# Kernel optimization log

Measured on AMD Instinct MI355X. Metric: run time of the kernel, lower is better.

## Reference

```python
import math
import jax, jax.numpy as jnp
import numpy as np

B, S, D = 4, 2048, 1024
H, HD = 16, 64
NUM_BUCKETS = 32
MAX_DISTANCE = 128
EPS = 1e-6
ENC_S = 512


def _relative_position_bucket(relative_position):
    # bidirectional=False path
    num_buckets = NUM_BUCKETS
    rp = -jnp.minimum(relative_position, 0)  # [S, S] nonneg
    max_exact = num_buckets // 2
    is_small = rp < max_exact
    scale = (num_buckets - max_exact) / math.log(MAX_DISTANCE / max_exact)
    large = max_exact + (jnp.log(jnp.maximum(rp, 1).astype(jnp.float32) / max_exact) * scale).astype(jnp.int32)
    large = jnp.minimum(large, num_buckets - 1)
    return jnp.where(is_small, rp, large)


def compute_bias(rel_emb, q_len, k_len):
    ctx = jnp.arange(q_len)[:, None]
    mem = jnp.arange(k_len)[None, :]
    bucket = _relative_position_bucket(mem - ctx)          # [q, k] int
    values = rel_emb[bucket]                                # [q, k, H]
    return jnp.transpose(values, (2, 0, 1))[None]           # [1, H, q, k]


def setup_inputs() -> dict:
    key = jax.random.key(0)
    ks = jax.random.split(key, 8)
    std = 0.02
    return {
        "input_ids": jax.random.normal(ks[0], (B, S, D), jnp.float32),
        "encoder_output": jax.random.normal(ks[1], (B, ENC_S, D), jnp.float32),
        "wq": jax.random.normal(ks[2], (D, H * HD), jnp.float32) * std,
        "wk": jax.random.normal(ks[3], (D, H * HD), jnp.float32) * std,
        "wv": jax.random.normal(ks[4], (D, H * HD), jnp.float32) * std,
        "wo": jax.random.normal(ks[5], (H * HD, D), jnp.float32) * std,
        "rel_emb": jax.random.normal(ks[6], (NUM_BUCKETS, H), jnp.float32) * std,
        "ln_w": jnp.ones((D,), jnp.float32),
    }


def reference(input_ids, encoder_output, wq, wk, wv, wo, rel_emb, ln_w):
    origin = input_ids
    # MT5LayerNorm: RMS norm, no mean subtraction, no bias
    variance = jnp.mean(jnp.square(input_ids.astype(jnp.float32)), axis=-1, keepdims=True)
    x = (input_ids * jax.lax.rsqrt(variance + EPS)) * ln_w

    q = (x @ wq).reshape(B, S, H, HD)
    k = (x @ wk).reshape(B, S, H, HD)
    v = (x @ wv).reshape(B, S, H, HD)

    # NOTE: T5-style attention has no 1/sqrt(d) scaling
    scores = jnp.einsum("bqhd,bkhd->bhqk", q, k)
    scores = scores + compute_bias(rel_emb, S, S)
    attn = jax.nn.softmax(scores, axis=-1)
    ctx = jnp.einsum("bhqk,bkhd->bqhd", attn, v).reshape(B, S, H * HD)
    attn_out = ctx @ wo

    # residual connection (dropout is identity at rate 0 / eval)
    return origin + attn_out
```

## Files before the change

### kernel.cpp

```cpp
#include <hip/hip_runtime.h>
#include <hip/hip_bf16.h>
#include <math.h>

#define S_LEN 2048
#define D_DIM 1024
#define NHEAD 16

typedef __attribute__((ext_vector_type(8))) short bf16x8;
typedef __attribute__((ext_vector_type(4))) float floatx4;

__device__ __forceinline__ short f32_bf16(float f) {
  union { float f; unsigned u; } v; v.f = f;
  unsigned r = v.u + 0x7FFFu + ((v.u >> 16) & 1u);
  return (short)(r >> 16);
}

__device__ __forceinline__ float exp2_fast(float x) {
#if __has_builtin(__builtin_amdgcn_exp2f)
  return __builtin_amdgcn_exp2f(x);
#else
  float r; asm("v_exp_f32 %0, %1" : "=v"(r) : "v"(x)); return r;
#endif
}

__device__ __forceinline__ void gload16(const void* g, void* l) {
  __builtin_amdgcn_global_load_lds((const __attribute__((address_space(1))) unsigned*)g,
                                   (__attribute__((address_space(3))) unsigned*)l,
                                   16, 0, 0);
}

__global__ __launch_bounds__(256) void prep_k(const float* __restrict__ x,
                                              const float* __restrict__ lnw,
                                              const float* __restrict__ wq,
                                              const float* __restrict__ wk,
                                              const float* __restrict__ wv,
                                              const float* __restrict__ wo,
                                              short* __restrict__ xb,
                                              short* __restrict__ oqkv,
                                              short* __restrict__ owo) {
  if (blockIdx.x < 8192) {
    int row = blockIdx.x;
    const float4* xr = (const float4*)(x + (size_t)row * D_DIM);
    float4 v = xr[threadIdx.x];
    float ss = v.x*v.x + v.y*v.y + v.z*v.z + v.w*v.w;
    #pragma unroll
    for (int off = 32; off > 0; off >>= 1) ss += __shfl_xor(ss, off);
    __shared__ float red[4];
    if ((threadIdx.x & 63) == 0) red[threadIdx.x >> 6] = ss;
    __syncthreads();
    float scale = rsqrtf((red[0]+red[1]+red[2]+red[3]) * (1.f/D_DIM) + 1e-6f);
    float4 wv4 = ((const float4*)lnw)[threadIdx.x];
    short4 o;
    o.x = f32_bf16(v.x*scale*wv4.x);
    o.y = f32_bf16(v.y*scale*wv4.y);
    o.z = f32_bf16(v.z*scale*wv4.z);
    o.w = f32_bf16(v.w*scale*wv4.w);
    ((short4*)xb)[(size_t)row*256 + threadIdx.x] = o;
  } else {
    int t = (blockIdx.x - 8192)*256 + threadIdx.x;
    if (t < 3072*1024) {
      int n = t >> 10, k = t & 1023;
      const float* src = (n < 1024) ? wq : ((n < 2048) ? wk : wv);
      float scale = (n < 1024) ? 1.44269504f : 1.0f;
      oqkv[t] = f32_bf16(src[(size_t)k*1024 + (n & 1023)] * scale);
    } else {
      int t2 = t - 3072*1024;
      int n = t2 >> 10, k = t2 & 1023;
      owo[t2] = f32_bf16(wo[(size_t)k*1024 + n]);
    }
  }
}

template<bool ADD_RES, int PANELS>
__global__ __launch_bounds__(256) void gemm_bt(const short* __restrict__ A,
                                               const short* __restrict__ Bt,
                                               short* __restrict__ Cb,
                                               float* __restrict__ Cf,
                                               const float* __restrict__ res,
                                               int M, int N, int K) {
  constexpr int BK = 32;
  __shared__ __align__(16) short As[2][128*BK];
  __shared__ __align__(16) short Bs[2][128*BK];
  int tid = threadIdx.x;
  int w = tid >> 6, lane = tid & 63, quad = lane >> 4, l16 = lane & 15;
  int wr = w >> 1, wc = w & 1;
  const int id = blockIdx.x;
  const int xcd = id & 7, g = id >> 3;
  const int bm = g / PANELS;
  const int bn = xcd * PANELS + (g % PANELS);
  const short* Ag = A + (size_t)bm * 128 * K;
  const short* Bg = Bt + (size_t)bn * 128 * K;
  const int r4 = lane >> 2;
  const int c4 = lane & 3;
  const int lc = c4 ^ (r4 & 3);
  const int swz = (quad ^ (l16 & 3)) * 8;

  floatx4 acc[4][4] = {};

  #define GSTAGE(p_, k0_) do {                                                  \
    _Pragma("unroll")                                                           \
    for (int i = 0; i < 2; i++) {                                               \
      int c = w + i*4;                                                          \
      gload16(Ag + (size_t)(c*16 + r4) * K + (k0_) + lc*8, &As[p_][c*16*BK]);   \
      gload16(Bg + (size_t)(c*16 + r4) * K + (k0_) + lc*8, &Bs[p_][c*16*BK]);   \
    }                                                                           \
  } while (0)

  GSTAGE(0, 0);
  int p = 0;
  for (int k0 = 0; k0 < K; k0 += BK) {
    __syncthreads();
    if (k0 + BK < K) GSTAGE(p ^ 1, k0 + BK);
    bf16x8 af[4], bfr[4];
    #pragma unroll
    for (int i = 0; i < 4; i++) {
      af[i]  = *(const bf16x8*)&As[p][(wr*64 + i*16 + l16)*BK + swz];
      bfr[i] = *(const bf16x8*)&Bs[p][(wc*64 + i*16 + l16)*BK + swz];
    }
    #pragma unroll
    for (int i = 0; i < 4; i++)
      #pragma unroll
      for (int j = 0; j < 4; j++)
        acc[i][j] = __builtin_amdgcn_mfma_f32_16x16x32_bf16(af[i], bfr[j], acc[i][j], 0, 0, 0);
    p ^= 1;
  }
  #undef GSTAGE

  #pragma unroll
  for (int i = 0; i < 4; i++) {
    int row0 = bm*128 + wr*64 + i*16 + quad*4;
    #pragma unroll
    for (int j = 0; j < 4; j++) {
      int col = bn*128 + wc*64 + j*16 + l16;
      #pragma unroll
      for (int r = 0; r < 4; r++) {
        size_t idx = (size_t)(row0 + r) * N + col;
        if (ADD_RES) Cf[idx] = res[idx] + acc[i][j][r];
        else         Cb[idx] = f32_bf16(acc[i][j][r]);
      }
    }
  }
}

__global__ __launch_bounds__(256) void pack_vt_k(const short* __restrict__ qkv,
                                                 short* __restrict__ vt) {
  __shared__ __align__(16) short tile[64][72];
  int s0 = blockIdx.x * 64;
  int bh = blockIdx.y;
  int b = bh >> 4, h = bh & 15;
  int t = threadIdx.x;
  #pragma unroll
  for (int i = 0; i < 2; i++) {
    int idx = t + i*256;
    int s = idx >> 3, c = idx & 7;
    *(bf16x8*)&tile[s][c*8] =
      *(const bf16x8*)&qkv[(size_t)(b*S_LEN + s0 + s)*3072 + 2048 + h*64 + c*8];
  }
  __syncthreads();
  #pragma unroll
  for (int i = 0; i < 2; i++) {
    int idx = t + i*256;
    int hd = idx >> 3, c = idx & 7;
    short tmp[8];
    #pragma unroll
    for (int j = 0; j < 8; j++) tmp[j] = tile[c*8 + j][hd];
    *(bf16x8*)&vt[((size_t)(bh*64 + hd))*S_LEN + s0 + c*8] = *(bf16x8*)tmp;
  }
}

__global__ __launch_bounds__(512) void flash_k(const short* __restrict__ qkv,
                                               const short* __restrict__ vt,
                                               const float* __restrict__ rel_emb,
                                               short* __restrict__ ctx) {
  __shared__ __align__(16) short Kb[2][64*64];
  __shared__ __align__(16) short Vb[2][64*64];
  __shared__ float lut2[132];

  const int L = blockIdx.x + 8*blockIdx.y;
  const int xcd = L & 7, kk_ = L >> 3;
  const int bh = xcd*8 + (kk_ >> 3);
  const int qt = kk_ & 7;
  const int b = bh >> 4, h = bh & 15;
  const int t = threadIdx.x, w = t >> 6, lane = t & 63, quad = lane >> 4, l16 = lane & 15;
  const float L2E = 1.44269504f;

  if (t < 129) {
    int rp = t, bucket;
    if (rp < 16) bucket = rp;
    else {
      bucket = 16 + (int)(logf((float)rp * 0.0625f) * (16.f / logf(8.f)));
      if (bucket > 31) bucket = 31;
    }
    lut2[t] = rel_emb[bucket*16 + h] * L2E;
  }
  const float bfut  = rel_emb[h] * L2E;
  const float bpast = rel_emb[31*16 + h] * L2E;
  const floatx4 bf4 = {bfut, bfut, bfut, bfut};
  const floatx4 bp4 = {bpast, bpast, bpast, bpast};
  const floatx4 zz4 = {0.f, 0.f, 0.f, 0.f};

  const int srow = lane >> 3;
  const int slc  = (lane & 7) ^ srow;
  const int rho  = w*8 + srow;
  const int kperm = 32*(rho >> 5) + 8*((rho >> 2) & 3) + 4*((rho >> 4) & 1) + (rho & 3);

  const short* kgU = qkv + ((size_t)b*S_LEN)*3072 + 1024 + h*64;
  const int    loK = kperm*3072 + slc*8;
  const short* vgU = vt + ((size_t)bh*64)*2048;
  const int    loV = rho*2048 + slc*8;

  bf16x8 qB[2][2];
  #pragma unroll
  for (int rb = 0; rb < 2; rb++) {
    const short* qb = qkv + ((size_t)(b*S_LEN + qt*256 + rb*128 + w*16 + l16))*3072 + h*64;
    qB[rb][0] = *(const bf16x8*)&qb[quad*8];
    qB[rb][1] = *(const bf16x8*)&qb[32 + quad*8];
  }

  floatx4 o[2][4] = {};
  floatx4 li4[2] = {};
  const short ONE = (short)0x3F80;
  bf16x8 onesA = {ONE, ONE, ONE, ONE, ONE, ONE, ONE, ONE};

  const int swz0 = (quad     ^ (l16 & 7)) * 8;
  const int swz1 = ((quad+4) ^ (l16 & 7)) * 8;

  #define STAGE(P_, KT_) do {                                                   \
    const short* ka_ = kgU + (size_t)(KT_)*196608 + loK;                        \
    gload16(ka_, &Kb[P_][(w*8)*64]);                                            \
    const short* va_ = vgU + loV + (KT_)*64;                                    \
    gload16(va_, &Vb[P_][(w*8)*64]);                                            \
  } while (0)

  #define BODY(P_, KT_) do {                                                    \
    __syncthreads();                                                            \
    if ((KT_) < 31) STAGE((P_) ^ 1, (KT_) + 1);      \
    bool boundary = ((KT_) >= 4*qt - 2) && ((KT_) <= 4*qt + 3);                 \
    floatx4 cinit = boundary ? zz4 : (((KT_) >= 4*qt) ? bf4 : bp4);             \
    floatx4 sc[2][4];                                                           \
    _Pragma("unroll")                                                           \
    for (int c = 0; c < 4; c++) {                                               \
      int rowA = (c*16 + l16)*64;                                               \
      bf16x8 ka0 = *(const bf16x8*)&Kb[P_][rowA + swz0];                        \
      bf16x8 ka1 = *(const bf16x8*)&Kb[P_][rowA + swz1];                        \
      _Pragma("unroll")                                                         \
      for (int rb = 0; rb < 2; rb++) {                                          \
        floatx4 z = __builtin_amdgcn_mfma_f32_16x16x32_bf16(ka0, qB[rb][0], cinit, 0, 0, 0); \
        z = __builtin_amdgcn_mfma_f32_16x16x32_bf16(ka1, qB[rb][1], z, 0, 0, 0);\
        sc[rb][c] = z;                                                          \
      }                                                                         \
    }                                                                           \
    if (boundary) {                                                             \
      _Pragma("unroll")                                                         \
      for (int rb = 0; rb < 2; rb++) {                                          \
        int q0 = qt*256 + rb*128 + w*16 + l16;                                  \
        _Pragma("unroll")                                                       \
        for (int c = 0; c < 4; c++) {                                           \
          int kk = (KT_)*64 + 32*(c >> 1) + 8*quad + 4*(c & 1);                 \
          _Pragma("unroll")                                                     \
          for (int r = 0; r < 4; r++) {                                         \
            int d = q0 - (kk + r);                                              \
            d = d < 0 ? 0 : (d > 128 ? 128 : d);                                \
            sc[rb][c][r] += lut2[d];                                            \
          }                                                                     \
        }                                                                       \
      }                                                                         \
    }                                                                           \
    _Pragma("unroll")                                                           \
    for (int rb = 0; rb < 2; rb++)                                              \
      _Pragma("unroll")                                                         \
      for (int c = 0; c < 4; c++)                                               \
        _Pragma("unroll")                                                       \
        for (int r = 0; r < 4; r++)                                             \
          sc[rb][c][r] = exp2_fast(sc[rb][c][r]);                               \
    bf16x8 pf[2][2];                                                            \
    _Pragma("unroll")                                                           \
    for (int rb = 0; rb < 2; rb++) {                                            \
      _Pragma("unroll")                                                         \
      for (int hh = 0; hh < 2; hh++) {                                          \
        union { bf16x8 v; unsigned u[4]; } pk;                                  \
        floatx4 a = sc[rb][2*hh], bb = sc[rb][2*hh + 1];                        \
        pk.u[0] = __builtin_amdgcn_perm(__float_as_uint(a[1]),  __float_as_uint(a[0]),  0x07060302); \
        pk.u[1] = __builtin_amdgcn_perm(__float_as_uint(a[3]),  __float_as_uint(a[2]),  0x07060302); \
        pk.u[2] = __builtin_amdgcn_perm(__float_as_uint(bb[1]), __float_as_uint(bb[0]), 0x07060302); \
        pk.u[3] = __builtin_amdgcn_perm(__float_as_uint(bb[3]), __float_as_uint(bb[2]), 0x07060302); \
        pf[rb][hh] = pk.v;                                                      \
      }                                                                         \
    }                                                                           \
    _Pragma("unroll")                                                           \
    for (int rb = 0; rb < 2; rb++) {                                            \
      li4[rb] = __builtin_amdgcn_mfma_f32_16x16x32_bf16(onesA, pf[rb][0], li4[rb], 0, 0, 0); \
      li4[rb] = __builtin_amdgcn_mfma_f32_16x16x32_bf16(onesA, pf[rb][1], li4[rb], 0, 0, 0); \
    }                                                                           \
    _Pragma("unroll")                                                           \
    for (int jj = 0; jj < 4; jj++) {                                            \
      int rowV = (jj*16 + l16)*64;                                              \
      bf16x8 va0 = *(const bf16x8*)&Vb[P_][rowV + swz0];                        \
      bf16x8 va1 = *(const bf16x8*)&Vb[P_][rowV + swz1];                        \
      _Pragma("unroll")                                                         \
      for (int rb = 0; rb < 2; rb++) {                                          \
        o[rb][jj] = __builtin_amdgcn_mfma_f32_16x16x32_bf16(va0, pf[rb][0], o[rb][jj], 0, 0, 0); \
        o[rb][jj] = __builtin_amdgcn_mfma_f32_16x16x32_bf16(va1, pf[rb][1], o[rb][jj], 0, 0, 0); \
      }                                                                         \
    }                                                                           \
  } while (0)

  STAGE(0, 0);
  for (int kt = 0; kt < 32; kt += 2) {
    BODY(0, kt);
    BODY(1, kt + 1);
  }

  #pragma unroll
  for (int rb = 0; rb < 2; rb++) {
    float inv = 1.f / li4[rb][0];
    size_t row = (size_t)(b*S_LEN + qt*256 + rb*128 + w*16 + l16);
    #pragma unroll
    for (int jj = 0; jj < 4; jj++) {
      short4 st;
      st.x = f32_bf16(o[rb][jj][0] * inv);
      st.y = f32_bf16(o[rb][jj][1] * inv);
      st.z = f32_bf16(o[rb][jj][2] * inv);
      st.w = f32_bf16(o[rb][jj][3] * inv);
      *(short4*)&ctx[row*1024 + h*64 + jj*16 + quad*4] = st;
    }
  }
  #undef STAGE
  #undef BODY
}

extern "C" void kernel_launch(void* const* d_in, const int* in_sizes, int n_in,
                              void* d_out, int out_size, void* d_ws, size_t ws_size,
                              hipStream_t stream) {
  const float* input_ids = (const float*)d_in[0];
  const float* wq      = (const float*)d_in[2];
  const float* wk      = (const float*)d_in[3];
  const float* wv      = (const float*)d_in[4];
  const float* wo      = (const float*)d_in[5];
  const float* rel_emb = (const float*)d_in[6];
  const float* ln_w    = (const float*)d_in[7];
  float* out = (float*)d_out;

  char* ws = (char*)d_ws;
  short* xb     = (short*)ws;  ws += (size_t)8192*1024*2;
  short* wqkv_t = (short*)ws;  ws += (size_t)3072*1024*2;
  short* wo_t   = (short*)ws;  ws += (size_t)1024*1024*2;
  short* qkv    = (short*)ws;  ws += (size_t)8192*3072*2;
  short* vt     = (short*)ws;  ws += (size_t)64*64*2048*2;
  short* ctx    = (short*)ws;  ws += (size_t)8192*1024*2;

  prep_k<<<8192 + 16384, 256, 0, stream>>>(input_ids, ln_w, wq, wk, wv, wo,
                                           xb, wqkv_t, wo_t);
  gemm_bt<false, 3><<<1536, 256, 0, stream>>>(xb, wqkv_t, qkv, nullptr, nullptr,
                                              8192, 3072, 1024);
  pack_vt_k<<<dim3(32, 64), 256, 0, stream>>>(qkv, vt);
  flash_k<<<dim3(8, 64), 512, 0, stream>>>(qkv, vt, rel_emb, ctx);
  gemm_bt<true, 1><<<512, 256, 0, stream>>>(ctx, wo_t, nullptr, out, input_ids,
                                            8192, 1024, 1024);
}
```

Before: 293.4 us.

## Fuse V transpose into QKV GEMM epilogue and tile weight conversion through LDS

The QKV GEMM's V-column blocks now write their tile straight into the transposed vt layout, so the separate pack_vt_k kernel and its read of V from qkv go away. The weight-conversion part of prep_k is rewritten as a 64x64 shared-memory tiled transpose with float4 loads and 16-byte bf16 stores, replacing the old one-element-per-thread strided gather. The trade-offs are that the vt stores from the epilogue are short4 writes strided by 2048 elements, less coalesced than before, and that V columns are no longer written to qkv.

Result: no change. 290.1 us (-1.1%).

```diff
diff --git a/kernel.cpp b/kernel.cpp
--- a/kernel.cpp
+++ b/kernel.cpp
@@ -57,26 +57,48 @@
     o.w = f32_bf16(v.w*scale*wv4.w);
     ((short4*)xb)[(size_t)row*256 + threadIdx.x] = o;
   } else {
-    int t = (blockIdx.x - 8192)*256 + threadIdx.x;
-    if (t < 3072*1024) {
-      int n = t >> 10, k = t & 1023;
-      const float* src = (n < 1024) ? wq : ((n < 2048) ? wk : wv);
-      float scale = (n < 1024) ? 1.44269504f : 1.0f;
-      oqkv[t] = f32_bf16(src[(size_t)k*1024 + (n & 1023)] * scale);
-    } else {
-      int t2 = t - 3072*1024;
-      int n = t2 >> 10, k = t2 & 1023;
-      owo[t2] = f32_bf16(wo[(size_t)k*1024 + n]);
-    }
-  }
-}
-
-template<bool ADD_RES, int PANELS>
+    __shared__ float tile[64][65];
+    int id = blockIdx.x - 8192;
+    int m  = id >> 8;
+    int tt = id & 255;
+    int tn = tt >> 4, tk = tt & 15;
+    const float* src = (m == 0) ? wq : (m == 1) ? wk : (m == 2) ? wv : wo;
+    float scale = (m == 0) ? 1.44269504f : 1.0f;
+    int t = threadIdx.x;
+    int kl  = t >> 4;
+    int nl4 = t & 15;
+    #pragma unroll
+    for (int i = 0; i < 4; i++) {
+      int k = i*16 + kl;
+      float4 v = *(const float4*)&src[(size_t)(tk*64 + k)*1024 + tn*64 + nl4*4];
+      tile[k][nl4*4+0] = v.x;
+      tile[k][nl4*4+1] = v.y;
+      tile[k][nl4*4+2] = v.z;
+      tile[k][nl4*4+3] = v.w;
+    }
+    __syncthreads();
+    short* dst = (m < 3) ? oqkv : owo;
+    size_t nbase = (m < 3) ? (size_t)m * 1024 : 0;
+    #pragma unroll
+    for (int i = 0; i < 2; i++) {
+      int idx = i*256 + t;
+      int nl = idx >> 3;
+      int g  = idx & 7;
+      short tmp[8];
+      #pragma unroll
+      for (int j = 0; j < 8; j++) tmp[j] = f32_bf16(tile[g*8 + j][nl] * scale);
+      *(bf16x8*)&dst[(nbase + tn*64 + nl)*1024 + tk*64 + g*8] = *(bf16x8*)tmp;
+    }
+  }
+}
+
+template<bool ADD_RES, int PANELS, bool WRITE_VT>
 __global__ __launch_bounds__(256) void gemm_bt(const short* __restrict__ A,
                                                const short* __restrict__ Bt,
                                                short* __restrict__ Cb,
                                                float* __restrict__ Cf,
                                                const float* __restrict__ res,
+                                               short* __restrict__ vt,
                                                int M, int N, int K) {
   constexpr int BK = 32;
   __shared__ __align__(16) short As[2][128*BK];
@@ -126,6 +148,26 @@
   }
   #undef GSTAGE
 
+  if (WRITE_VT && bn >= 16) {
+    #pragma unroll
+    for (int i = 0; i < 4; i++) {
+      int row0 = bm*128 + wr*64 + i*16 + quad*4;
+      int b = row0 >> 11, s = row0 & 2047;
+      #pragma unroll
+      for (int j = 0; j < 4; j++) {
+        int hcol = bn*128 + wc*64 + j*16 + l16 - 2048;
+        short4 st;
+        st.x = f32_bf16(acc[i][j][0]);
+        st.y = f32_bf16(acc[i][j][1]);
+        st.z = f32_bf16(acc[i][j][2]);
+        st.w = f32_bf16(acc[i][j][3]);
+        int bh = (b << 4) + (hcol >> 6);
+        *(short4*)&vt[((size_t)(bh*64 + (hcol & 63)))*2048 + s] = st;
+      }
+    }
+    return;
+  }
+
   #pragma unroll
   for (int i = 0; i < 4; i++) {
     int row0 = bm*128 + wr*64 + i*16 + quad*4;
@@ -139,32 +181,6 @@
         else         Cb[idx] = f32_bf16(acc[i][j][r]);
       }
     }
-  }
-}
-
-__global__ __launch_bounds__(256) void pack_vt_k(const short* __restrict__ qkv,
-                                                 short* __restrict__ vt) {
-  __shared__ __align__(16) short tile[64][72];
-  int s0 = blockIdx.x * 64;
-  int bh = blockIdx.y;
-  int b = bh >> 4, h = bh & 15;
-  int t = threadIdx.x;
-  #pragma unroll
-  for (int i = 0; i < 2; i++) {
-    int idx = t + i*256;
-    int s = idx >> 3, c = idx & 7;
-    *(bf16x8*)&tile[s][c*8] =
-      *(const bf16x8*)&qkv[(size_t)(b*S_LEN + s0 + s)*3072 + 2048 + h*64 + c*8];
-  }
-  __syncthreads();
-  #pragma unroll
-  for (int i = 0; i < 2; i++) {
-    int idx = t + i*256;
-    int hd = idx >> 3, c = idx & 7;
-    short tmp[8];
-    #pragma unroll
-    for (int j = 0; j < 8; j++) tmp[j] = tile[c*8 + j][hd];
-    *(bf16x8*)&vt[((size_t)(bh*64 + hd))*S_LEN + s0 + c*8] = *(bf16x8*)tmp;
   }
 }
 
@@ -349,12 +365,11 @@
   short* vt     = (short*)ws;  ws += (size_t)64*64*2048*2;
   short* ctx    = (short*)ws;  ws += (size_t)8192*1024*2;
 
-  prep_k<<<8192 + 16384, 256, 0, stream>>>(input_ids, ln_w, wq, wk, wv, wo,
-                                           xb, wqkv_t, wo_t);
-  gemm_bt<false, 3><<<1536, 256, 0, stream>>>(xb, wqkv_t, qkv, nullptr, nullptr,
-                                              8192, 3072, 1024);
-  pack_vt_k<<<dim3(32, 64), 256, 0, stream>>>(qkv, vt);
+  prep_k<<<8192 + 1024, 256, 0, stream>>>(input_ids, ln_w, wq, wk, wv, wo,
+                                          xb, wqkv_t, wo_t);
+  gemm_bt<false, 3, true><<<1536, 256, 0, stream>>>(xb, wqkv_t, qkv, nullptr,
+                                                    nullptr, vt, 8192, 3072, 1024);
   flash_k<<<dim3(8, 64), 512, 0, stream>>>(qkv, vt, rel_emb, ctx);
-  gemm_bt<true, 1><<<512, 256, 0, stream>>>(ctx, wo_t, nullptr, out, input_ids,
-                                            8192, 1024, 1024);
-}
+  gemm_bt<true, 1, false><<<512, 256, 0, stream>>>(ctx, wo_t, nullptr, out,
+                                                   input_ids, nullptr, 8192, 1024, 1024);
+}
```
